# Kernel optimization log

Hardware: AMD Instinct MI355X
Metric: run time of the kernel (lower is better)

## Reference

```python
import jax, jax.numpy as jnp
import numpy as np
import math

# Static config (matches init_kwargs)
H = 1024      # hidden_dim
F = 2048      # ffn_dim
E = 32        # num_experts
K = 2         # num_selected_experts (top-k)
CAP_FACTOR = 4.0
AUX_COEF = 0.01
B, S = 2, 2048
T = B * S
CAP = max(int(CAP_FACTOR * T / E), 4)  # expert capacity per GPT5MoERouter


def setup_inputs() -> dict:
    key = jax.random.key(0)
    k_x, k_r, k_g, k_u, k_d = jax.random.split(key, 5)
    expert_scale = 1.0 / math.sqrt(2.0 * 8)
    std_gu = 0.02 * expert_scale / math.sqrt(2.0)
    std_d = 0.02 * expert_scale / math.sqrt(2.0 * 3)
    x = jax.random.normal(k_x, (B, S, H), dtype=jnp.float32)
    Wr = jax.random.normal(k_r, (E, H), dtype=jnp.float32) * (0.02 / math.sqrt(2.0 * H))
    br = jnp.full((E,), -math.log(E), dtype=jnp.float32)
    Wg = jax.random.normal(k_g, (E, H, F), dtype=jnp.float32) * std_gu
    Wu = jax.random.normal(k_u, (E, H, F), dtype=jnp.float32) * std_gu
    Wd = jax.random.normal(k_d, (E, F, H), dtype=jnp.float32) * std_d
    return {"x": x, "Wr": Wr, "br": br, "Wg": Wg, "Wu": Wu, "Wd": Wd}


def reference(x, Wr, br, Wg, Wu, Wd):
    xf = x.reshape(T, H)
    # --- Router: softmax in fp32, top-k, renormalize selected weights ---
    logits = xf @ Wr.T + br                                   # [T, E]
    probs = jax.nn.softmax(logits.astype(jnp.float32), axis=-1)
    w, idx = jax.lax.top_k(probs, K)                          # [T, K]
    w = jax.nn.softmax(w, axis=-1)
    # --- Capacity-bounded dispatch (token-major, first-come priority) ---
    e_flat = idx.reshape(-1)                                  # [T*K]
    oh = jax.nn.one_hot(e_flat, E, dtype=jnp.int32)           # [T*K, E]
    pos = ((jnp.cumsum(oh, axis=0) - oh) * oh).sum(-1)        # slot within expert
    keep = pos < CAP
    posc = jnp.where(keep, pos, 0)
    xk = jnp.repeat(xf, K, axis=0) * keep[:, None].astype(x.dtype)  # [T*K, H]
    buf = jnp.zeros((E, CAP, H), x.dtype).at[e_flat, posc].add(xk)  # [E, C, H]
    # --- Fused SwiGLU experts (grouped GEMMs) ---
    g = jnp.einsum('ech,ehf->ecf', buf, Wg)
    u = jnp.einsum('ech,ehf->ecf', buf, Wu)
    hid = jax.nn.silu(g) * u
    y = jnp.einsum('ecf,efh->ech', hid, Wd)                   # [E, C, H]
    # --- Combine: gather back and weight by renormalized router probs ---
    yk = y[e_flat, posc] * (keep[:, None].astype(x.dtype) * w.reshape(-1)[:, None])
    out = yk.reshape(T, K, H).sum(1).reshape(B, S, H)
    # --- Load-balancing aux loss (top-1 utilization, per router code) ---
    router_prob_per_expert = probs.mean(0)                    # [E]
    util = jax.nn.one_hot(idx[:, 0], E, dtype=jnp.float32).mean(0)
    aux_loss = jnp.sum(router_prob_per_expert * util) * E * AUX_COEF
    return out, aux_loss
```

## Files before the change

### kernel.cpp

```cpp
#include <hip/hip_runtime.h>

#define NEXP 32
#define HD   1024
#define FD   2048
#define NTOK 4096
#define CAP  512

typedef __attribute__((ext_vector_type(8))) short s8v;
typedef __attribute__((ext_vector_type(4))) float f4v;

__device__ __forceinline__ unsigned short f2bf(float f) {
  unsigned u = __float_as_uint(f);
  u += 0x7fffu + ((u >> 16) & 1u);
  return (unsigned short)(u >> 16);
}
__device__ __forceinline__ float bf2f(unsigned short h) {
  return __uint_as_float(((unsigned)h) << 16);
}

__global__ __launch_bounds__(256) void router_kernel(
    const float* __restrict__ x, const float* __restrict__ Wr, const float* __restrict__ br,
    int* __restrict__ eidx, float* __restrict__ wts,
    float* __restrict__ probs_sum, int* __restrict__ cnt1)
{
  const int wid = threadIdx.x >> 6, lane = threadIdx.x & 63;
  const int t0 = blockIdx.x * 16 + wid * 4;
  __shared__ float ll[4][4][NEXP];
  __shared__ float ps[NEXP];
  __shared__ int   c1[NEXP];
  if (threadIdx.x < NEXP) { ps[threadIdx.x] = 0.f; c1[threadIdx.x] = 0; }
  __syncthreads();

  float xr[4][16];
  #pragma unroll
  for (int tk = 0; tk < 4; tk++) {
    const float* xp = x + (size_t)(t0 + tk) * HD + lane * 4;
    #pragma unroll
    for (int i = 0; i < 4; i++) {
      float4 v = *(const float4*)(xp + i * 256);
      xr[tk][i*4+0]=v.x; xr[tk][i*4+1]=v.y; xr[tk][i*4+2]=v.z; xr[tk][i*4+3]=v.w;
    }
  }
  for (int e = 0; e < NEXP; e++) {
    const float* wp = Wr + e * HD + lane * 4;
    float w[16];
    #pragma unroll
    for (int i = 0; i < 4; i++) {
      float4 v = *(const float4*)(wp + i * 256);
      w[i*4+0]=v.x; w[i*4+1]=v.y; w[i*4+2]=v.z; w[i*4+3]=v.w;
    }
    float s0=0.f,s1=0.f,s2=0.f,s3=0.f;
    #pragma unroll
    for (int i = 0; i < 16; i++) {
      s0 += xr[0][i]*w[i]; s1 += xr[1][i]*w[i];
      s2 += xr[2][i]*w[i]; s3 += xr[3][i]*w[i];
    }
    #pragma unroll
    for (int o = 32; o > 0; o >>= 1) {
      s0 += __shfl_xor(s0, o); s1 += __shfl_xor(s1, o);
      s2 += __shfl_xor(s2, o); s3 += __shfl_xor(s3, o);
    }
    if (lane == 0) {
      float b = br[e];
      ll[wid][0][e]=s0+b; ll[wid][1][e]=s1+b; ll[wid][2][e]=s2+b; ll[wid][3][e]=s3+b;
    }
  }
  __syncthreads();

  for (int tk = 0; tk < 4; tk++) {
    const int t = t0 + tk;
    float lg[NEXP];
    #pragma unroll
    for (int e = 0; e < NEXP; e++) lg[e] = ll[wid][tk][e];
    float mx = lg[0];
    #pragma unroll
    for (int e = 1; e < NEXP; e++) mx = fmaxf(mx, lg[e]);
    float pr[NEXP]; float den = 0.f;
    #pragma unroll
    for (int e = 0; e < NEXP; e++) { pr[e] = __expf(lg[e] - mx); den += pr[e]; }
    float inv = 1.f / den;
    #pragma unroll
    for (int e = 0; e < NEXP; e++) pr[e] *= inv;
    int i1 = 0; float l1 = lg[0];
    #pragma unroll
    for (int e = 1; e < NEXP; e++) if (lg[e] > l1) { l1 = lg[e]; i1 = e; }
    int i2 = (i1 == 0) ? 1 : 0; float l2 = lg[i2];
    #pragma unroll
    for (int e = 0; e < NEXP; e++) if (e != i1 && lg[e] > l2) { l2 = lg[e]; i2 = e; }
    if (lane == 0) {
      float p1 = pr[i1], p2 = pr[i2];
      float ex = __expf(p2 - p1);
      float w1 = 1.f / (1.f + ex);
      eidx[2*t] = i1; eidx[2*t+1] = i2;
      wts[2*t] = w1;  wts[2*t+1] = ex * w1;
      atomicAdd(&c1[i1], 1);
    }
    if (lane < NEXP) atomicAdd(&ps[lane], pr[lane]);
  }
  __syncthreads();
  if (threadIdx.x < NEXP) {
    atomicAdd(&probs_sum[threadIdx.x], ps[threadIdx.x]);
    atomicAdd(&cnt1[threadIdx.x], c1[threadIdx.x]);
  }
}

__global__ __launch_bounds__(256) void scan_kernel(
    const int* __restrict__ eidx, int* __restrict__ pos,
    int* __restrict__ slot_tok, int* __restrict__ cnt)
{
  __shared__ int lc[256 * NEXP];
  const int tid = threadIdx.x;
  const int base = tid * NEXP;
  #pragma unroll
  for (int e = 0; e < NEXP; e++) lc[base + e] = 0;
  for (int j = 0; j < 32; j++) lc[base + eidx[tid * 32 + j]]++;
  __syncthreads();
  if (tid < NEXP) {
    int run = 0;
    for (int j = 0; j < 256; j++) {
      int v = lc[j * NEXP + tid];
      lc[j * NEXP + tid] = run;
      run += v;
    }
    cnt[tid] = run;
  }
  __syncthreads();
  for (int j = 0; j < 32; j++) {
    const int i = tid * 32 + j;
    const int e = eidx[i];
    const int p = lc[base + e]++;
    pos[i] = p;
    if (p < CAP) slot_tok[e * CAP + p] = i >> 1;
  }
}

__global__ __launch_bounds__(256) void gather_kernel(
    const float* __restrict__ x, const int* __restrict__ slot_tok,
    const int* __restrict__ cnt, unsigned short* __restrict__ Xe)
{
  const int e = blockIdx.y, row = blockIdx.x;
  const int ne = min(cnt[e], CAP);
  const int npad = (ne + 127) & ~127;
  if (row >= npad) return;
  const int h = threadIdx.x * 4;
  unsigned short* dst = Xe + ((size_t)e * CAP + row) * HD + h;
  if (row < ne) {
    const int t = slot_tok[e * CAP + row];
    float4 v = *(const float4*)(x + (size_t)t * HD + h);
    ushort4 o; o.x = f2bf(v.x); o.y = f2bf(v.y); o.z = f2bf(v.z); o.w = f2bf(v.w);
    *(ushort4*)dst = o;
  } else {
    *(ushort4*)dst = make_ushort4(0, 0, 0, 0);
  }
}

template<int NMAT, int KDIM, int NDIM>
__global__ __launch_bounds__(256, 1) void gemm_kernel(
    const unsigned short* __restrict__ A, const float* __restrict__ B0,
    const float* __restrict__ B1, unsigned short* __restrict__ C,
    const int* __restrict__ cnt)
{
  const int e  = blockIdx.z;
  const int m0 = blockIdx.y * 128;
  const int n0 = blockIdx.x * 128;
  const int ne = min(cnt[e], CAP);
  if (m0 >= ne) return;

  __shared__ __align__(16) unsigned short As[128][40];
  __shared__ __align__(16) unsigned short Bs[NMAT][128][40];
  __shared__ __align__(16) unsigned short Bst[NMAT][32][136];

  const int tid = threadIdx.x;
  const int lane = tid & 63;
  const int wid = tid >> 6;
  const int wm = (wid >> 1) * 64, wn = (wid & 1) * 64;

  f4v acc[NMAT][4][4];
  #pragma unroll
  for (int m = 0; m < NMAT; m++)
    #pragma unroll
    for (int i = 0; i < 4; i++)
      #pragma unroll
      for (int j = 0; j < 4; j++)
        acc[m][i][j] = (f4v){0.f, 0.f, 0.f, 0.f};

  const unsigned short* Ae = A + ((size_t)e * CAP + m0) * KDIM;
  const float* bp0 = B0 + (size_t)e * KDIM * NDIM + n0;
  const float* bp1 = (NMAT == 2) ? (B1 + (size_t)e * KDIM * NDIM + n0) : bp0;

  for (int k0 = 0; k0 < KDIM; k0 += 32) {
    #pragma unroll
    for (int mat = 0; mat < NMAT; mat++) {
      const float* bp = ((mat == 0) ? bp0 : bp1) + (size_t)k0 * NDIM;
      #pragma unroll
      for (int s = 0; s < 4; s++) {
        const int c = tid + 256 * s;
        const int kk = c >> 5, n4 = (c & 31) * 4;
        float4 v = *(const float4*)(bp + kk * NDIM + n4);
        uint2 pk;
        pk.x = f2bf(v.x) | ((unsigned)f2bf(v.y) << 16);
        pk.y = f2bf(v.z) | ((unsigned)f2bf(v.w) << 16);
        *(uint2*)&Bst[mat][kk][n4] = pk;
      }
    }
    __syncthreads();
    #pragma unroll
    for (int s = 0; s < 2; s++) {
      const int c = tid + 256 * s;
      const int row = c >> 2, cc = (c & 3) * 8;
      uint4 v = *(const uint4*)(Ae + (size_t)row * KDIM + k0 + cc);
      *(uint4*)&As[row][cc] = v;
    }
    #pragma unroll
    for (int mat = 0; mat < NMAT; mat++) {
      #pragma unroll
      for (int s = 0; s < 2; s++) {
        const int task = tid + 256 * s;
        const int n = task & 127, oct = (task >> 7) * 8;
        unsigned v0 = Bst[mat][oct+0][n] | ((unsigned)Bst[mat][oct+1][n] << 16);
        unsigned v1 = Bst[mat][oct+2][n] | ((unsigned)Bst[mat][oct+3][n] << 16);
        unsigned v2 = Bst[mat][oct+4][n] | ((unsigned)Bst[mat][oct+5][n] << 16);
        unsigned v3 = Bst[mat][oct+6][n] | ((unsigned)Bst[mat][oct+7][n] << 16);
        *(uint4*)&Bs[mat][n][oct] = make_uint4(v0, v1, v2, v3);
      }
    }
    __syncthreads();
    s8v af[4];
    #pragma unroll
    for (int fm = 0; fm < 4; fm++)
      af[fm] = *(const s8v*)&As[wm + fm * 16 + (lane & 15)][(lane >> 4) * 8];
    #pragma unroll
    for (int mat = 0; mat < NMAT; mat++) {
      #pragma unroll
      for (int fn = 0; fn < 4; fn++) {
        s8v bfr = *(const s8v*)&Bs[mat][wn + fn * 16 + (lane & 15)][(lane >> 4) * 8];
        #pragma unroll
        for (int fm = 0; fm < 4; fm++)
          acc[mat][fm][fn] = __builtin_amdgcn_mfma_f32_16x16x32_bf16(
              af[fm], bfr, acc[mat][fm][fn], 0, 0, 0);
      }
    }
  }

  const int roff = (lane >> 4) * 4, coff = lane & 15;
  #pragma unroll
  for (int fm = 0; fm < 4; fm++) {
    #pragma unroll
    for (int fn = 0; fn < 4; fn++) {
      #pragma unroll
      for (int r = 0; r < 4; r++) {
        const int row = m0 + wm + fm * 16 + roff + r;
        const int col = n0 + wn + fn * 16 + coff;
        float val;
        if (NMAT == 2) {
          float g = acc[0][fm][fn][r], u = acc[1][fm][fn][r];
          val = (g / (1.f + __expf(-g))) * u;
        } else {
          val = acc[0][fm][fn][r];
        }
        C[((size_t)e * CAP + row) * NDIM + col] = f2bf(val);
      }
    }
  }
}

__global__ __launch_bounds__(256) void combine_kernel(
    const unsigned short* __restrict__ y, const int* __restrict__ eidx,
    const float* __restrict__ wts, const int* __restrict__ pos,
    const float* __restrict__ ps, const int* __restrict__ c1,
    float* __restrict__ out)
{
  const int t = blockIdx.x;
  const int h = threadIdx.x * 4;
  float a0 = 0.f, a1 = 0.f, a2 = 0.f, a3 = 0.f;
  #pragma unroll
  for (int k = 0; k < 2; k++) {
    const int i = 2 * t + k;
    const int p = pos[i];
    if (p < CAP) {
      const int e = eidx[i];
      const float w = wts[i];
      ushort4 v = *(const ushort4*)(y + ((size_t)e * CAP + p) * HD + h);
      a0 += w * bf2f(v.x); a1 += w * bf2f(v.y);
      a2 += w * bf2f(v.z); a3 += w * bf2f(v.w);
    }
  }
  *(float4*)(out + (size_t)t * HD + h) = make_float4(a0, a1, a2, a3);
  if (t == 0 && threadIdx.x == 0) {
    float a = 0.f;
    for (int e = 0; e < NEXP; e++) a += ps[e] * (float)c1[e];
    out[(size_t)NTOK * HD] = a * (32.f * 0.01f / (4096.f * 4096.f));
  }
}

extern "C" void kernel_launch(void* const* d_in, const int* in_sizes, int n_in,
                              void* d_out, int out_size, void* d_ws, size_t ws_size,
                              hipStream_t stream) {
  const float* x  = (const float*)d_in[0];
  const float* Wr = (const float*)d_in[1];
  const float* br = (const float*)d_in[2];
  const float* Wg = (const float*)d_in[3];
  const float* Wu = (const float*)d_in[4];
  const float* Wd = (const float*)d_in[5];
  float* out = (float*)d_out;

  char* ws = (char*)d_ws;
  unsigned short* Xe  = (unsigned short*)(ws);
  unsigned short* hid = (unsigned short*)(ws + 33554432);
  unsigned short* yb  = (unsigned short*)(ws + 100663296);
  int*   eidx = (int*)  (ws + 134217728);
  float* wts  = (float*)(ws + 134250496);
  int*   pos  = (int*)  (ws + 134283264);
  int*   slot = (int*)  (ws + 134316032);
  int*   cnt  = (int*)  (ws + 134381568);
  float* ps   = (float*)(ws + 134381696);
  int*   c1   = (int*)  (ws + 134381824);

  hipMemsetAsync(ws + 134381696, 0, 256, stream);

  router_kernel<<<256, 256, 0, stream>>>(x, Wr, br, eidx, wts, ps, c1);
  scan_kernel<<<1, 256, 0, stream>>>(eidx, pos, slot, cnt);
  gather_kernel<<<dim3(CAP, NEXP), 256, 0, stream>>>(x, slot, cnt, Xe);
  gemm_kernel<2, HD, FD><<<dim3(FD / 128, CAP / 128, NEXP), 256, 0, stream>>>(
      Xe, Wg, Wu, hid, cnt);
  gemm_kernel<1, FD, HD><<<dim3(HD / 128, CAP / 128, NEXP), 256, 0, stream>>>(
      hid, Wd, nullptr, yb, cnt);
  combine_kernel<<<NTOK, 256, 0, stream>>>(yb, eidx, wts, pos, ps, c1, out);
}
```

Measured before the change: 1.173 ms.

## Pre-transpose expert weights to bf16 and load GEMM tiles via global_load_lds

```diff
diff --git a/kernel.cpp b/kernel.cpp
--- a/kernel.cpp
+++ b/kernel.cpp
@@ -16,6 +16,44 @@
 }
 __device__ __forceinline__ float bf2f(unsigned short h) {
   return __uint_as_float(((unsigned)h) << 16);
+}
+
+#define GLL16(gp, lp) __builtin_amdgcn_global_load_lds( \
+    (const __attribute__((address_space(1))) unsigned int*)(gp), \
+    (__attribute__((address_space(3))) unsigned int*)(lp), 16, 0, 0)
+
+template<int K, int N>
+__global__ __launch_bounds__(256) void transpose_kernel(
+    const float* __restrict__ in, unsigned short* __restrict__ outp)
+{
+  __shared__ unsigned short lds[64 * 66];
+  const int e = blockIdx.z;
+  const int k0 = blockIdx.y * 64, n0 = blockIdx.x * 64;
+  const float* ip = in + (size_t)e * K * N + (size_t)k0 * N + n0;
+  unsigned short* op = outp + (size_t)e * N * K + (size_t)n0 * K + k0;
+  const int t = threadIdx.x;
+  const int kk = t >> 4, nn = (t & 15) * 4;
+  #pragma unroll
+  for (int i = 0; i < 4; i++) {
+    const int k = kk + i * 16;
+    float4 v = *(const float4*)(ip + (size_t)k * N + nn);
+    uint2 pk;
+    pk.x = f2bf(v.x) | ((unsigned)f2bf(v.y) << 16);
+    pk.y = f2bf(v.z) | ((unsigned)f2bf(v.w) << 16);
+    *(uint2*)&lds[k * 66 + nn] = pk;
+  }
+  __syncthreads();
+  const int n_r = t >> 4, k4 = (t & 15) * 4;
+  #pragma unroll
+  for (int i = 0; i < 4; i++) {
+    const int n = n_r + i * 16;
+    ushort4 o;
+    o.x = lds[(k4 + 0) * 66 + n];
+    o.y = lds[(k4 + 1) * 66 + n];
+    o.z = lds[(k4 + 2) * 66 + n];
+    o.w = lds[(k4 + 3) * 66 + n];
+    *(ushort4*)(op + (size_t)n * K + k4) = o;
+  }
 }
 
 __global__ __launch_bounds__(256) void router_kernel(
@@ -154,114 +192,98 @@
   }
 }
 
-template<int NMAT, int KDIM, int NDIM>
-__global__ __launch_bounds__(256, 1) void gemm_kernel(
-    const unsigned short* __restrict__ A, const float* __restrict__ B0,
-    const float* __restrict__ B1, unsigned short* __restrict__ C,
+template<int NMAT, int KDIM, int NDIM, int TN>
+__global__ __launch_bounds__(256) void gemm_kernel(
+    const unsigned short* __restrict__ A, const unsigned short* __restrict__ B0,
+    const unsigned short* __restrict__ B1, unsigned short* __restrict__ C,
     const int* __restrict__ cnt)
 {
-  const int e  = blockIdx.z;
-  const int m0 = blockIdx.y * 128;
-  const int n0 = blockIdx.x * 128;
+  constexpr int FN = TN / 32;
+  const int e = blockIdx.z;
   const int ne = min(cnt[e], CAP);
+  const int m0 = blockIdx.x * 128;
   if (m0 >= ne) return;
-
-  __shared__ __align__(16) unsigned short As[128][40];
-  __shared__ __align__(16) unsigned short Bs[NMAT][128][40];
-  __shared__ __align__(16) unsigned short Bst[NMAT][32][136];
+  const int n0 = blockIdx.y * TN;
+
+  __shared__ __align__(16) unsigned short As[128 * 64];
+  __shared__ __align__(16) unsigned short Bs[NMAT][TN * 64];
 
   const int tid = threadIdx.x;
-  const int lane = tid & 63;
-  const int wid = tid >> 6;
-  const int wm = (wid >> 1) * 64, wn = (wid & 1) * 64;
-
-  f4v acc[NMAT][4][4];
+  const int lane = tid & 63, wid = tid >> 6;
+  const int wm = (wid >> 1) * 64;
+  const int wn = (wid & 1) * (TN / 2);
+  const int l8 = lane >> 3;
+  const int gch = (lane & 7) ^ l8;
+  const int quad = lane >> 4, fr = lane & 15, x7 = lane & 7;
+
+  f4v acc[NMAT][4][FN];
   #pragma unroll
   for (int m = 0; m < NMAT; m++)
     #pragma unroll
     for (int i = 0; i < 4; i++)
       #pragma unroll
-      for (int j = 0; j < 4; j++)
+      for (int j = 0; j < FN; j++)
         acc[m][i][j] = (f4v){0.f, 0.f, 0.f, 0.f};
 
-  const unsigned short* Ae = A + ((size_t)e * CAP + m0) * KDIM;
-  const float* bp0 = B0 + (size_t)e * KDIM * NDIM + n0;
-  const float* bp1 = (NMAT == 2) ? (B1 + (size_t)e * KDIM * NDIM + n0) : bp0;
-
-  for (int k0 = 0; k0 < KDIM; k0 += 32) {
+  const unsigned short* Ae  = A  + ((size_t)e * CAP + m0) * KDIM;
+  const unsigned short* Bp0 = B0 + ((size_t)e * NDIM + n0) * KDIM;
+  const unsigned short* Bp1 = B1 + ((size_t)e * NDIM + n0) * KDIM;
+
+  for (int k0 = 0; k0 < KDIM; k0 += 64) {
+    #pragma unroll
+    for (int j = 0; j < 4; j++) {
+      const int r = wid * 32 + j * 8 + l8;
+      GLL16(Ae + (size_t)r * KDIM + k0 + gch * 8, &As[(wid * 32 + j * 8) * 64]);
+    }
     #pragma unroll
     for (int mat = 0; mat < NMAT; mat++) {
-      const float* bp = ((mat == 0) ? bp0 : bp1) + (size_t)k0 * NDIM;
-      #pragma unroll
-      for (int s = 0; s < 4; s++) {
-        const int c = tid + 256 * s;
-        const int kk = c >> 5, n4 = (c & 31) * 4;
-        float4 v = *(const float4*)(bp + kk * NDIM + n4);
-        uint2 pk;
-        pk.x = f2bf(v.x) | ((unsigned)f2bf(v.y) << 16);
-        pk.y = f2bf(v.z) | ((unsigned)f2bf(v.w) << 16);
-        *(uint2*)&Bst[mat][kk][n4] = pk;
+      const unsigned short* Bp = mat ? Bp1 : Bp0;
+      #pragma unroll
+      for (int j = 0; j < TN / 32; j++) {
+        const int r = wid * (TN / 4) + j * 8 + l8;
+        GLL16(Bp + (size_t)r * KDIM + k0 + gch * 8,
+              &Bs[mat][(wid * (TN / 4) + j * 8) * 64]);
       }
     }
     __syncthreads();
     #pragma unroll
-    for (int s = 0; s < 2; s++) {
-      const int c = tid + 256 * s;
-      const int row = c >> 2, cc = (c & 3) * 8;
-      uint4 v = *(const uint4*)(Ae + (size_t)row * KDIM + k0 + cc);
-      *(uint4*)&As[row][cc] = v;
-    }
-    #pragma unroll
-    for (int mat = 0; mat < NMAT; mat++) {
-      #pragma unroll
-      for (int s = 0; s < 2; s++) {
-        const int task = tid + 256 * s;
-        const int n = task & 127, oct = (task >> 7) * 8;
-        unsigned v0 = Bst[mat][oct+0][n] | ((unsigned)Bst[mat][oct+1][n] << 16);
-        unsigned v1 = Bst[mat][oct+2][n] | ((unsigned)Bst[mat][oct+3][n] << 16);
-        unsigned v2 = Bst[mat][oct+4][n] | ((unsigned)Bst[mat][oct+5][n] << 16);
-        unsigned v3 = Bst[mat][oct+6][n] | ((unsigned)Bst[mat][oct+7][n] << 16);
-        *(uint4*)&Bs[mat][n][oct] = make_uint4(v0, v1, v2, v3);
-      }
+    for (int kc = 0; kc < 2; kc++) {
+      const int pos8 = ((kc * 4 + quad) ^ x7) * 8;
+      s8v af[4];
+      #pragma unroll
+      for (int fm = 0; fm < 4; fm++)
+        af[fm] = *(const s8v*)&As[(wm + fm * 16 + fr) * 64 + pos8];
+      #pragma unroll
+      for (int mat = 0; mat < NMAT; mat++)
+        #pragma unroll
+        for (int fn = 0; fn < FN; fn++) {
+          s8v bfr = *(const s8v*)&Bs[mat][(wn + fn * 16 + fr) * 64 + pos8];
+          #pragma unroll
+          for (int fm = 0; fm < 4; fm++)
+            acc[mat][fm][fn] = __builtin_amdgcn_mfma_f32_16x16x32_bf16(
+                af[fm], bfr, acc[mat][fm][fn], 0, 0, 0);
+        }
     }
     __syncthreads();
-    s8v af[4];
-    #pragma unroll
-    for (int fm = 0; fm < 4; fm++)
-      af[fm] = *(const s8v*)&As[wm + fm * 16 + (lane & 15)][(lane >> 4) * 8];
-    #pragma unroll
-    for (int mat = 0; mat < NMAT; mat++) {
-      #pragma unroll
-      for (int fn = 0; fn < 4; fn++) {
-        s8v bfr = *(const s8v*)&Bs[mat][wn + fn * 16 + (lane & 15)][(lane >> 4) * 8];
-        #pragma unroll
-        for (int fm = 0; fm < 4; fm++)
-          acc[mat][fm][fn] = __builtin_amdgcn_mfma_f32_16x16x32_bf16(
-              af[fm], bfr, acc[mat][fm][fn], 0, 0, 0);
-      }
-    }
-  }
-
-  const int roff = (lane >> 4) * 4, coff = lane & 15;
-  #pragma unroll
-  for (int fm = 0; fm < 4; fm++) {
-    #pragma unroll
-    for (int fn = 0; fn < 4; fn++) {
+  }
+
+  #pragma unroll
+  for (int fm = 0; fm < 4; fm++)
+    #pragma unroll
+    for (int fn = 0; fn < FN; fn++)
       #pragma unroll
       for (int r = 0; r < 4; r++) {
-        const int row = m0 + wm + fm * 16 + roff + r;
-        const int col = n0 + wn + fn * 16 + coff;
-        float val;
+        const int row = m0 + wm + fm * 16 + quad * 4 + r;
+        const int col = n0 + wn + fn * 16 + fr;
+        float v;
         if (NMAT == 2) {
           float g = acc[0][fm][fn][r], u = acc[1][fm][fn][r];
-          val = (g / (1.f + __expf(-g))) * u;
+          v = (g / (1.f + __expf(-g))) * u;
         } else {
-          val = acc[0][fm][fn][r];
+          v = acc[0][fm][fn][r];
         }
-        C[((size_t)e * CAP + row) * NDIM + col] = f2bf(val);
+        C[((size_t)e * CAP + row) * NDIM + col] = f2bf(v);
       }
-    }
-  }
 }
 
 __global__ __launch_bounds__(256) void combine_kernel(
@@ -305,25 +327,36 @@
   float* out = (float*)d_out;
 
   char* ws = (char*)d_ws;
-  unsigned short* Xe  = (unsigned short*)(ws);
-  unsigned short* hid = (unsigned short*)(ws + 33554432);
-  unsigned short* yb  = (unsigned short*)(ws + 100663296);
-  int*   eidx = (int*)  (ws + 134217728);
-  float* wts  = (float*)(ws + 134250496);
-  int*   pos  = (int*)  (ws + 134283264);
-  int*   slot = (int*)  (ws + 134316032);
-  int*   cnt  = (int*)  (ws + 134381568);
-  float* ps   = (float*)(ws + 134381696);
-  int*   c1   = (int*)  (ws + 134381824);
-
-  hipMemsetAsync(ws + 134381696, 0, 256, stream);
-
-  router_kernel<<<256, 256, 0, stream>>>(x, Wr, br, eidx, wts, ps, c1);
+  const size_t MB = 1048576;
+  unsigned short* WT0 = (unsigned short*)(ws);
+  unsigned short* WT1 = (unsigned short*)(ws + 128 * MB);
+  unsigned short* Xe  = (unsigned short*)(ws + 256 * MB);
+  unsigned short* hid = (unsigned short*)(ws + 288 * MB);
+  unsigned short* yb  = (unsigned short*)(ws + 352 * MB);
+  char* sm = ws + 384 * MB;
+  int*   eidx = (int*)  (sm);
+  float* wts  = (float*)(sm + 32768);
+  int*   pos  = (int*)  (sm + 65536);
+  int*   slot = (int*)  (sm + 98304);
+  int*   cnt  = (int*)  (sm + 163840);
+  float* ps   = (float*)(sm + 163968);
+  int*   c1   = (int*)  (sm + 164096);
+
+  hipMemsetAsync(sm + 163968, 0, 256, stream);
+
+  transpose_kernel<HD, FD><<<dim3(FD/64, HD/64, NEXP), 256, 0, stream>>>(Wg, WT0);
+  transpose_kernel<HD, FD><<<dim3(FD/64, HD/64, NEXP), 256, 0, stream>>>(Wu, WT1);
+
+  router_kernel<<<NTOK/16, 256, 0, stream>>>(x, Wr, br, eidx, wts, ps, c1);
   scan_kernel<<<1, 256, 0, stream>>>(eidx, pos, slot, cnt);
   gather_kernel<<<dim3(CAP, NEXP), 256, 0, stream>>>(x, slot, cnt, Xe);
-  gemm_kernel<2, HD, FD><<<dim3(FD / 128, CAP / 128, NEXP), 256, 0, stream>>>(
-      Xe, Wg, Wu, hid, cnt);
-  gemm_kernel<1, FD, HD><<<dim3(HD / 128, CAP / 128, NEXP), 256, 0, stream>>>(
-      hid, Wd, nullptr, yb, cnt);
+
+  gemm_kernel<2, HD, FD, 64><<<dim3(CAP/128, FD/64, NEXP), 256, 0, stream>>>(
+      Xe, WT0, WT1, hid, cnt);
+
+  transpose_kernel<FD, HD><<<dim3(HD/64, FD/64, NEXP), 256, 0, stream>>>(Wd, WT0);
+  gemm_kernel<1, FD, HD, 128><<<dim3(CAP/128, HD/128, NEXP), 256, 0, stream>>>(
+      hid, WT0, WT0, yb, cnt);
+
   combine_kernel<<<NTOK, 256, 0, stream>>>(yb, eidx, wts, pos, ps, c1, out);
 }
```

After: 1.108 ms. 5.5% less time.
